# Optimization experiments

Hardware: AMD Instinct MI355X
Metric: run time of the kernel (lower is better)

The kernel has to match this reference:

```python
import jax, jax.numpy as jnp
import numpy as np

H = 1024
EPS = 1e-5
N_ENT = 1000
TOP_K = 5


def _ln(x, g, b):
    mu = jnp.mean(x, axis=-1, keepdims=True)
    var = jnp.mean((x - mu) ** 2, axis=-1, keepdims=True)
    return (x - mu) * jax.lax.rsqrt(var + EPS) * g + b


def _gelu(x):
    return jax.nn.gelu(x, approximate=False)  # torch nn.GELU default (erf)


def setup_inputs() -> dict:
    key = jax.random.key(0)
    ks = jax.random.split(key, 24)
    s = 0.02
    inp = {
        'hidden_states': jax.random.normal(ks[0], (8, 2048, H), jnp.float32),
        'entity_embeddings': jax.random.normal(ks[1], (N_ENT, H), jnp.float32) * 0.01,
        # entity_encoder: H -> 2H -> H -> LN
        'ee_w1': jax.random.normal(ks[2], (H, 2 * H), jnp.float32) * s,
        'ee_b1': jnp.zeros((2 * H,), jnp.float32),
        'ee_w2': jax.random.normal(ks[3], (2 * H, H), jnp.float32) * s,
        'ee_b2': jnp.zeros((H,), jnp.float32),
        'ee_g': jnp.ones((H,), jnp.float32),
        'ee_beta': jnp.zeros((H,), jnp.float32),
        # relation_encoder: H -> H -> H -> LN
        're_w1': jax.random.normal(ks[4], (H, H), jnp.float32) * s,
        're_b1': jnp.zeros((H,), jnp.float32),
        're_w2': jax.random.normal(ks[5], (H, H), jnp.float32) * s,
        're_b2': jnp.zeros((H,), jnp.float32),
        're_g': jnp.ones((H,), jnp.float32),
        're_beta': jnp.zeros((H,), jnp.float32),
        # reasoning_network: 3H -> 2H -> H -> LN
        'rn_w1': jax.random.normal(ks[6], (3 * H, 2 * H), jnp.float32) * s,
        'rn_b1': jnp.zeros((2 * H,), jnp.float32),
        'rn_w2': jax.random.normal(ks[7], (2 * H, H), jnp.float32) * s,
        'rn_b2': jnp.zeros((H,), jnp.float32),
        'rn_g': jnp.ones((H,), jnp.float32),
        'rn_beta': jnp.zeros((H,), jnp.float32),
        # validation_network: H -> H/2 -> 1 -> sigmoid
        'vn_w1': jax.random.normal(ks[8], (H, H // 2), jnp.float32) * s,
        'vn_b1': jnp.zeros((H // 2,), jnp.float32),
        'vn_w2': jax.random.normal(ks[9], (H // 2, 1), jnp.float32) * s,
        'vn_b2': jnp.zeros((1,), jnp.float32),
    }
    return inp


def reference(hidden_states, entity_embeddings,
              ee_w1, ee_b1, ee_w2, ee_b2, ee_g, ee_beta,
              re_w1, re_b1, re_w2, re_b2, re_g, re_beta,
              rn_w1, rn_b1, rn_w2, rn_b2, rn_g, rn_beta,
              vn_w1, vn_b1, vn_w2, vn_b2):
    # entity encoder over all tokens: [B,S,H]
    entity_features = _ln(_gelu(hidden_states @ ee_w1 + ee_b1) @ ee_w2 + ee_b2, ee_g, ee_beta)

    # query=None path: relation encoder on mean-pooled hidden states [B,H]
    pooled = jnp.mean(hidden_states, axis=1)
    relation_features = _ln(_gelu(pooled @ re_w1 + re_b1) @ re_w2 + re_b2, re_g, re_beta)
    query_features = relation_features

    # similarity + top-k entity retrieval
    entity_similarities = query_features @ entity_embeddings.T  # [B, N_ENT]
    top_values, top_indices = jax.lax.top_k(entity_similarities, TOP_K)
    retrieved_entities = entity_embeddings[top_indices]  # [B, K, H]

    # reasoning input: [mean retrieved entity | relation | mean context]
    entity_vec = jnp.mean(retrieved_entities, axis=1)  # [B,H]
    context_vec = jnp.mean(hidden_states, axis=1)      # [B,H]
    reasoning_in = jnp.concatenate([entity_vec, relation_features, context_vec], axis=-1)  # [B,3H]
    reasoning_output = _ln(_gelu(reasoning_in @ rn_w1 + rn_b1) @ rn_w2 + rn_b2, rn_g, rn_beta)

    validation_scores = jax.nn.sigmoid(_gelu(reasoning_output @ vn_w1 + vn_b1) @ vn_w2 + vn_b2)

    return (entity_features, relation_features, retrieved_entities,
            entity_similarities, top_indices, reasoning_output, validation_scores)
```

## Files before the change

### kernel.cpp

```cpp
#include <hip/hip_runtime.h>
#include <math.h>

#define H 1024
#define SEQ 2048
#define BATCH 8
#define N_ENT 1000
#define TOPK 5
#define LN_EPS 1e-5f

using bf16x8 = __attribute__((ext_vector_type(8))) __bf16;
using f32x4  = __attribute__((ext_vector_type(4))) float;
#define AS1 __attribute__((address_space(1)))
#define AS3 __attribute__((address_space(3)))


__device__ __forceinline__ float gelu_erf(float x) {
    return 0.5f * x * (1.0f + erff(x * 0.70710678118654752440f));
}

__device__ __forceinline__ float sigmoidf_(float x) {
    return 1.0f / (1.0f + expf(-x));
}

__device__ __forceinline__ unsigned short f2bf(float f) {
    unsigned int u = __float_as_uint(f);
    unsigned int r = (u + 0x7fffu + ((u >> 16) & 1u)) >> 16;
    return (unsigned short)r;
}

__device__ float block_sum(float v, float* red) {
    for (int off = 32; off > 0; off >>= 1) v += __shfl_down(v, off, 64);
    int wid = threadIdx.x >> 6;
    int lane = threadIdx.x & 63;
    int nw = blockDim.x >> 6;
    if (lane == 0) red[wid] = v;
    __syncthreads();
    if (threadIdx.x == 0) {
        float s = 0.f;
        for (int i = 0; i < nw; ++i) s += red[i];
        red[0] = s;
    }
    __syncthreads();
    float r = red[0];
    __syncthreads();
    return r;
}


__global__ void f2bf_kernel(const float* __restrict__ in, unsigned short* __restrict__ out, int n) {
    int i = (blockIdx.x * blockDim.x + threadIdx.x) * 4;
    if (i >= n) return;
    float4 v = *(const float4*)(in + i);
    ushort4 o;
    o.x = f2bf(v.x); o.y = f2bf(v.y); o.z = f2bf(v.z); o.w = f2bf(v.w);
    *(ushort4*)(out + i) = o;
}

__global__ void transpose_bf_kernel(const float* __restrict__ in, unsigned short* __restrict__ out,
                                    int R, int C) {
    __shared__ float tile[32][33];
    int c0 = blockIdx.x * 32, r0 = blockIdx.y * 32;
    int tx = threadIdx.x & 31, ty = threadIdx.x >> 5;
#pragma unroll
    for (int i = 0; i < 32; i += 8)
        tile[ty + i][tx] = in[(size_t)(r0 + ty + i) * C + c0 + tx];
    __syncthreads();
#pragma unroll
    for (int i = 0; i < 32; i += 8)
        out[(size_t)(c0 + ty + i) * R + r0 + tx] = f2bf(tile[tx][ty + i]);
}


__global__ void pool1_kernel(const float* __restrict__ hs, float* __restrict__ part) {
    int sc = blockIdx.x, b = blockIdx.y, t = threadIdx.x;
    float a0 = 0, a1 = 0, a2 = 0, a3 = 0;
    const float* p = hs + ((size_t)b * SEQ + sc * 64) * H;
    for (int s = 0; s < 64; ++s) {
        const float* q = p + (size_t)s * H;
        a0 += q[t]; a1 += q[t + 256]; a2 += q[t + 512]; a3 += q[t + 768];
    }
    float* o = part + ((size_t)b * 32 + sc) * H;
    o[t] = a0; o[t + 256] = a1; o[t + 512] = a2; o[t + 768] = a3;
}

__global__ void pool2_kernel(const float* __restrict__ part, float* __restrict__ pooled) {
    int b = blockIdx.x, t = threadIdx.x;
    for (int c = 0; c < 4; ++c) {
        float s = 0.f;
        for (int sc = 0; sc < 32; ++sc) s += part[((size_t)b * 32 + sc) * H + t + c * 256];
        pooled[b * H + t + c * 256] = s * (1.0f / SEQ);
    }
}


template <int KRANGE>
__global__ void mlp_partial_kernel(const float* __restrict__ X, int ldx,
                                   const float* __restrict__ W, int N,
                                   float* __restrict__ part) {
    __shared__ float xs[8][KRANGE];
    int jb = blockIdx.x, ks = blockIdx.y, t = threadIdx.x;
    int k0 = ks * KRANGE;
    for (int i = t; i < 8 * KRANGE; i += 256) {
        int b = i / KRANGE, k = i % KRANGE;
        xs[b][k] = X[(size_t)b * ldx + k0 + k];
    }
    __syncthreads();
    int j = jb * 256 + t;
    float acc[8] = {};
    for (int k = 0; k < KRANGE; ++k) {
        float w = W[(size_t)(k0 + k) * N + j];
#pragma unroll
        for (int b = 0; b < 8; ++b) acc[b] = fmaf(xs[b][k], w, acc[b]);
    }
#pragma unroll
    for (int b = 0; b < 8; ++b) part[((size_t)ks * 8 + b) * N + j] = acc[b];
}

__global__ void mlp_reduce_gelu_kernel(const float* __restrict__ part, const float* __restrict__ bias,
                                       float* __restrict__ out, int N, int nks) {
    int b = blockIdx.y;
    int j = blockIdx.x * 256 + threadIdx.x;
    float s = bias[j];
    for (int ks = 0; ks < nks; ++ks) s += part[((size_t)ks * 8 + b) * N + j];
    out[(size_t)b * N + j] = gelu_erf(s);
}

__global__ void mlp_reduce_ln_kernel(const float* __restrict__ part, const float* __restrict__ bias,
                                     const float* __restrict__ g, const float* __restrict__ be,
                                     float* __restrict__ out, int nks) {
    __shared__ float red[32];
    int b = blockIdx.x, t = threadIdx.x;
    float s = bias[t];
    for (int ks = 0; ks < nks; ++ks) s += part[((size_t)ks * 8 + b) * H + t];
    float mu = block_sum(s, red) * (1.0f / H);
    float d = s - mu;
    float var = block_sum(d * d, red) * (1.0f / H);
    out[(size_t)b * H + t] = d * rsqrtf(var + LN_EPS) * g[t] + be[t];
}


__global__ void sim_kernel(const float* __restrict__ rel, const float* __restrict__ ent,
                           float* __restrict__ sims) {
    __shared__ float rl[8 * H];
    int t = threadIdx.x;
    for (int i = t; i < 8 * H; i += 256) rl[i] = rel[i];
    __syncthreads();
    int e = blockIdx.x * 4 + (t >> 6);
    int lane = t & 63;
    float ev[16];
    const float* ep = ent + (size_t)e * H;
#pragma unroll
    for (int i = 0; i < 16; ++i) ev[i] = ep[lane + i * 64];
#pragma unroll
    for (int b = 0; b < 8; ++b) {
        float a = 0.f;
#pragma unroll
        for (int i = 0; i < 16; ++i) a = fmaf(ev[i], rl[b * H + lane + i * 64], a);
        for (int off = 32; off > 0; off >>= 1) a += __shfl_down(a, off, 64);
        if (lane == 0) sims[b * N_ENT + e] = a;
    }
}

__global__ void topk_kernel(const float* __restrict__ sims, float* __restrict__ out_idx_f,
                            int* __restrict__ idx_i) {
    __shared__ float v[1024];
    __shared__ float rv[4];
    __shared__ int ri[4];
    int b = blockIdx.x, t = threadIdx.x;
    for (int i = t; i < 1024; i += 256) v[i] = (i < N_ENT) ? sims[b * N_ENT + i] : -INFINITY;
    __syncthreads();
    for (int k = 0; k < TOPK; ++k) {
        float best = -INFINITY;
        int bi = 0x7fffffff;
        for (int i = t; i < 1024; i += 256) {
            float x = v[i];
            if (x > best || (x == best && i < bi)) { best = x; bi = i; }
        }
        for (int off = 32; off > 0; off >>= 1) {
            float ov = __shfl_down(best, off, 64);
            int oi = __shfl_down(bi, off, 64);
            if (ov > best || (ov == best && oi < bi)) { best = ov; bi = oi; }
        }
        if ((t & 63) == 0) { rv[t >> 6] = best; ri[t >> 6] = bi; }
        __syncthreads();
        if (t == 0) {
            for (int w = 1; w < 4; ++w)
                if (rv[w] > rv[0] || (rv[w] == rv[0] && ri[w] < ri[0])) { rv[0] = rv[w]; ri[0] = ri[w]; }
            int sel = ri[0];
            out_idx_f[b * TOPK + k] = (float)sel;
            idx_i[b * TOPK + k] = sel;
            v[sel] = -INFINITY;
        }
        __syncthreads();
    }
}

__global__ void gather_kernel(const float* __restrict__ ent, const int* __restrict__ idx,
                              float* __restrict__ retrieved, float* __restrict__ evec) {
    int b = blockIdx.x, h = threadIdx.x;
    float acc = 0.f;
    for (int k = 0; k < TOPK; ++k) {
        float v = ent[(size_t)idx[b * TOPK + k] * H + h];
        retrieved[((size_t)b * TOPK + k) * H + h] = v;
        acc += v;
    }
    evec[b * H + h] = acc * (1.0f / TOPK);
}

__global__ void concat_kernel(const float* __restrict__ evec, const float* __restrict__ rel,
                              const float* __restrict__ pooled, float* __restrict__ xin) {
    int b = blockIdx.x, t = threadIdx.x;
    xin[(size_t)b * 3 * H + t] = evec[b * H + t];
    xin[(size_t)b * 3 * H + H + t] = rel[b * H + t];
    xin[(size_t)b * 3 * H + 2 * H + t] = pooled[b * H + t];
}

__global__ void vn_final_kernel(const float* __restrict__ part, const float* __restrict__ b1,
                                const float* __restrict__ w2, const float* __restrict__ b2,
                                float* __restrict__ vs, int nks) {
    __shared__ float red[32];
    int b = blockIdx.x, t = threadIdx.x;
    float s = b1[t];
    for (int ks = 0; ks < nks; ++ks) s += part[((size_t)ks * 8 + b) * 512 + t];
    float c = gelu_erf(s) * w2[t];
    float tot = block_sum(c, red);
    if (t == 0) vs[b] = sigmoidf_(tot + b2[0]);
}

template <int GELU_BF16_OUT>
__global__ __launch_bounds__(256) void gemm_mfma(const unsigned short* __restrict__ A,
                                                 const unsigned short* __restrict__ Bt,
                                                 const float* __restrict__ bias,
                                                 void* __restrict__ Cout,
                                                 int M, int N, int K) {
    __shared__ __align__(16) unsigned short As[128 * 32];
    __shared__ __align__(16) unsigned short Bs[128 * 32];
    const int tid = threadIdx.x;
    const int lane = tid & 63;
    const int m0 = blockIdx.y * 128, n0 = blockIdx.x * 128;
    const int wave = tid >> 6;
    const int wm = (wave >> 1) * 64, wn = (wave & 1) * 64;

    const int rowA_f = wm + (lane & 15);
    const int rowB_f = wn + (lane & 15);
    const int kq = (lane >> 4) * 8;

    f32x4 acc[4][4] = {};

    for (int k0 = 0; k0 < K; k0 += 32) {
#pragma unroll
        for (int r = 0; r < 2; ++r) {
            int e = (r * 256 + tid) * 8;
            int row = e >> 5, kk = e & 31;
            const unsigned short* ga = A + (size_t)(m0 + row) * K + k0 + kk;
            const unsigned short* gb = Bt + (size_t)(n0 + row) * K + k0 + kk;
            unsigned short* la = As + (size_t)(r * 256 + (tid & ~63)) * 8;
            unsigned short* lb = Bs + (size_t)(r * 256 + (tid & ~63)) * 8;
            __builtin_amdgcn_global_load_lds((AS1 void*)ga, (AS3 void*)la, 16, 0, 0);
            __builtin_amdgcn_global_load_lds((AS1 void*)gb, (AS3 void*)lb, 16, 0, 0);
        }
        __syncthreads();
        bf16x8 af[4], bfg[4];
#pragma unroll
        for (int i = 0; i < 4; ++i)
            af[i] = *(const bf16x8*)(As + (rowA_f + i * 16) * 32 + kq);
#pragma unroll
        for (int j = 0; j < 4; ++j)
            bfg[j] = *(const bf16x8*)(Bs + (rowB_f + j * 16) * 32 + kq);
#pragma unroll
        for (int i = 0; i < 4; ++i)
#pragma unroll
            for (int j = 0; j < 4; ++j)
                acc[i][j] = __builtin_amdgcn_mfma_f32_16x16x32_bf16(af[i], bfg[j], acc[i][j], 0, 0, 0);
        __syncthreads();
    }

    const int cn = lane & 15;
    const int rbase = (lane >> 4) * 4;
#pragma unroll
    for (int i = 0; i < 4; ++i) {
#pragma unroll
        for (int j = 0; j < 4; ++j) {
            int n = n0 + wn + j * 16 + cn;
            float bv = bias[n];
            int mb = m0 + wm + i * 16 + rbase;
#pragma unroll
            for (int r = 0; r < 4; ++r) {
                float c = acc[i][j][r] + bv;
                if (GELU_BF16_OUT) {
                    c = gelu_erf(c);
                    ((unsigned short*)Cout)[(size_t)(mb + r) * N + n] = f2bf(c);
                } else {
                    ((float*)Cout)[(size_t)(mb + r) * N + n] = c;
                }
            }
        }
    }
}

__global__ void ln_rows_kernel(float* __restrict__ x, const float* __restrict__ g,
                               const float* __restrict__ beta) {
    __shared__ float red[32];
    float* p = x + (size_t)blockIdx.x * H;
    int t = threadIdx.x;
    float v[4];
#pragma unroll
    for (int i = 0; i < 4; ++i) v[i] = p[t + i * 256];
    float s = v[0] + v[1] + v[2] + v[3];
    float mu = block_sum(s, red) * (1.0f / H);
    float d2 = 0.f;
#pragma unroll
    for (int i = 0; i < 4; ++i) { float d = v[i] - mu; d2 += d * d; }
    float var = block_sum(d2, red) * (1.0f / H);
    float inv = rsqrtf(var + LN_EPS);
#pragma unroll
    for (int i = 0; i < 4; ++i)
        p[t + i * 256] = (v[i] - mu) * inv * g[t + i * 256] + beta[t + i * 256];
}


extern "C" void kernel_launch(void* const* d_in, const int* in_sizes, int n_in,
                              void* d_out, int out_size, void* d_ws, size_t ws_size,
                              hipStream_t stream) {
    const float* hs     = (const float*)d_in[0];
    const float* ent    = (const float*)d_in[1];
    const float* ee_w1  = (const float*)d_in[2];
    const float* ee_b1  = (const float*)d_in[3];
    const float* ee_w2  = (const float*)d_in[4];
    const float* ee_b2  = (const float*)d_in[5];
    const float* ee_g   = (const float*)d_in[6];
    const float* ee_be  = (const float*)d_in[7];
    const float* re_w1  = (const float*)d_in[8];
    const float* re_b1  = (const float*)d_in[9];
    const float* re_w2  = (const float*)d_in[10];
    const float* re_b2  = (const float*)d_in[11];
    const float* re_g   = (const float*)d_in[12];
    const float* re_be  = (const float*)d_in[13];
    const float* rn_w1  = (const float*)d_in[14];
    const float* rn_b1  = (const float*)d_in[15];
    const float* rn_w2  = (const float*)d_in[16];
    const float* rn_b2  = (const float*)d_in[17];
    const float* rn_g   = (const float*)d_in[18];
    const float* rn_be  = (const float*)d_in[19];
    const float* vn_w1  = (const float*)d_in[20];
    const float* vn_b1  = (const float*)d_in[21];
    const float* vn_w2  = (const float*)d_in[22];
    const float* vn_b2  = (const float*)d_in[23];

    float* out = (float*)d_out;
    float* ef   = out;
    float* rel  = ef + (size_t)BATCH * SEQ * H;
    float* retr = rel + BATCH * H;
    float* sims = retr + BATCH * TOPK * H;
    float* tidx = sims + BATCH * N_ENT;
    float* ro   = tidx + BATCH * TOPK;
    float* vs   = ro + BATCH * H;

    float* ws = (float*)d_ws;
    size_t o = 0;
    float* pooled = ws + o; o += 8192;
    float* evec   = ws + o; o += 8192;
    int*   idx_i  = (int*)(ws + o); o += 64;
    float* xin    = ws + o; o += 8 * 3 * H;
    float* h1r    = ws + o; o += 8 * H;
    float* h1n    = ws + o; o += 8 * 2 * H;
    float* part   = ws + o; o += 24 * 8 * 2048;
    unsigned short* w1t = (unsigned short*)(ws + o); o += (2048 * 1024) / 2;
    unsigned short* w2t = (unsigned short*)(ws + o); o += (2048 * 1024) / 2;
    unsigned short* hsb = (unsigned short*)(ws + o);

    long long avail = (long long)(ws_size / 4) - (long long)o;
    int chunk = (int)(avail / 1536);
    chunk &= ~127;
    if (chunk > BATCH * SEQ) chunk = BATCH * SEQ;
    if (chunk < 128) chunk = 128;
    unsigned short* midb = hsb + (size_t)chunk * H;

    transpose_bf_kernel<<<dim3(2048 / 32, 1024 / 32), 256, 0, stream>>>(ee_w1, w1t, 1024, 2048);
    transpose_bf_kernel<<<dim3(1024 / 32, 2048 / 32), 256, 0, stream>>>(ee_w2, w2t, 2048, 1024);

    pool1_kernel<<<dim3(32, BATCH), 256, 0, stream>>>(hs, part);
    pool2_kernel<<<BATCH, 256, 0, stream>>>(part, pooled);

    mlp_partial_kernel<64><<<dim3(4, 16), 256, 0, stream>>>(pooled, H, re_w1, H, part);
    mlp_reduce_gelu_kernel<<<dim3(4, 8), 256, 0, stream>>>(part, re_b1, h1r, H, 16);
    mlp_partial_kernel<64><<<dim3(4, 16), 256, 0, stream>>>(h1r, H, re_w2, H, part);
    mlp_reduce_ln_kernel<<<BATCH, 1024, 0, stream>>>(part, re_b2, re_g, re_be, rel, 16);

    sim_kernel<<<250, 256, 0, stream>>>(rel, ent, sims);
    topk_kernel<<<BATCH, 256, 0, stream>>>(sims, tidx, idx_i);
    gather_kernel<<<BATCH, 1024, 0, stream>>>(ent, idx_i, retr, evec);
    concat_kernel<<<BATCH, 1024, 0, stream>>>(evec, rel, pooled, xin);

    mlp_partial_kernel<128><<<dim3(8, 24), 256, 0, stream>>>(xin, 3 * H, rn_w1, 2 * H, part);
    mlp_reduce_gelu_kernel<<<dim3(8, 8), 256, 0, stream>>>(part, rn_b1, h1n, 2 * H, 24);
    mlp_partial_kernel<128><<<dim3(4, 16), 256, 0, stream>>>(h1n, 2 * H, rn_w2, H, part);
    mlp_reduce_ln_kernel<<<BATCH, 1024, 0, stream>>>(part, rn_b2, rn_g, rn_be, ro, 16);

    mlp_partial_kernel<128><<<dim3(2, 8), 256, 0, stream>>>(ro, H, vn_w1, 512, part);
    vn_final_kernel<<<BATCH, 512, 0, stream>>>(part, vn_b1, vn_w2, vn_b2, vs, 8);

    int total = BATCH * SEQ;
    for (int r0 = 0; r0 < total; r0 += chunk) {
        int m = total - r0;
        if (m > chunk) m = chunk;
        int nconv = m * H;
        f2bf_kernel<<<(nconv / 4 + 255) / 256, 256, 0, stream>>>(hs + (size_t)r0 * H, hsb, nconv);
        gemm_mfma<1><<<dim3(2048 / 128, m / 128), 256, 0, stream>>>(hsb, w1t, ee_b1, midb,
                                                                    m, 2048, 1024);
        gemm_mfma<0><<<dim3(1024 / 128, m / 128), 256, 0, stream>>>(midb, w2t, ee_b2,
                                                                    ef + (size_t)r0 * H,
                                                                    m, 1024, 2048);
    }
    ln_rows_kernel<<<total, 256, 0, stream>>>(ef, ee_g, ee_be);
}
```

Before: 600.2 us.

## Fuse bf16 conversion into pooling, add fast GELU, remap GEMM grid, vectorize LN

When the workspace holds the whole activation, the pooling kernel now also writes the bf16 copy of hidden_states, so the separate f2bf pass and its second read of the input are dropped. The erf-based GELU is replaced by a polynomial approximation using hardware rcp/exp2, the gather and concat kernels are merged, and pool2 gets more blocks. The GEMM grid is flattened with M as the fastest-varying index so blocks that share a weight tile run together for better cache reuse, and the row LayerNorm uses float4 accesses. The erf approximation adds small numerical error, and the pooling kernel now does extra scalar 2-byte stores.

```diff
diff --git a/kernel.cpp b/kernel.cpp
--- a/kernel.cpp
+++ b/kernel.cpp
@@ -14,8 +14,15 @@
 #define AS3 __attribute__((address_space(3)))
 
 
-__device__ __forceinline__ float gelu_erf(float x) {
-    return 0.5f * x * (1.0f + erff(x * 0.70710678118654752440f));
+__device__ __forceinline__ float gelu_fast(float x) {
+    float z = fabsf(x) * 0.70710678118654752440f;
+    float t = __builtin_amdgcn_rcpf(fmaf(0.3275911f, z, 1.0f));
+    float p = fmaf(fmaf(fmaf(fmaf(1.061405429f, t, -1.453152027f), t, 1.421413741f),
+                        t, -0.284496736f), t, 0.254829592f) * t;
+    float e = __builtin_amdgcn_exp2f(-z * z * 1.44269504088896f);
+    float erfz = fmaf(-p, e, 1.0f);
+    float s = copysignf(erfz, x);
+    return 0.5f * x * (1.0f + s);
 }
 
 __device__ __forceinline__ float sigmoidf_(float x) {
@@ -71,25 +78,30 @@
 }
 
 
-__global__ void pool1_kernel(const float* __restrict__ hs, float* __restrict__ part) {
+__global__ void pool1_kernel(const float* __restrict__ hs, float* __restrict__ part,
+                             unsigned short* __restrict__ hsb) {
     int sc = blockIdx.x, b = blockIdx.y, t = threadIdx.x;
     float a0 = 0, a1 = 0, a2 = 0, a3 = 0;
-    const float* p = hs + ((size_t)b * SEQ + sc * 64) * H;
+    size_t rowbase = (size_t)b * SEQ + sc * 64;
+    const float* p = hs + rowbase * H;
     for (int s = 0; s < 64; ++s) {
         const float* q = p + (size_t)s * H;
-        a0 += q[t]; a1 += q[t + 256]; a2 += q[t + 512]; a3 += q[t + 768];
+        float v0 = q[t], v1 = q[t + 256], v2 = q[t + 512], v3 = q[t + 768];
+        a0 += v0; a1 += v1; a2 += v2; a3 += v3;
+        if (hsb) {
+            unsigned short* w = hsb + (rowbase + s) * H;
+            w[t] = f2bf(v0); w[t + 256] = f2bf(v1); w[t + 512] = f2bf(v2); w[t + 768] = f2bf(v3);
+        }
     }
     float* o = part + ((size_t)b * 32 + sc) * H;
     o[t] = a0; o[t + 256] = a1; o[t + 512] = a2; o[t + 768] = a3;
 }
 
 __global__ void pool2_kernel(const float* __restrict__ part, float* __restrict__ pooled) {
-    int b = blockIdx.x, t = threadIdx.x;
-    for (int c = 0; c < 4; ++c) {
-        float s = 0.f;
-        for (int sc = 0; sc < 32; ++sc) s += part[((size_t)b * 32 + sc) * H + t + c * 256];
-        pooled[b * H + t + c * 256] = s * (1.0f / SEQ);
-    }
+    int b = blockIdx.y, c = blockIdx.x, t = threadIdx.x;
+    float s = 0.f;
+    for (int sc = 0; sc < 32; ++sc) s += part[((size_t)b * 32 + sc) * H + t + c * 256];
+    pooled[b * H + t + c * 256] = s * (1.0f / SEQ);
 }
 
 
@@ -122,7 +134,7 @@
     int j = blockIdx.x * 256 + threadIdx.x;
     float s = bias[j];
     for (int ks = 0; ks < nks; ++ks) s += part[((size_t)ks * 8 + b) * N + j];
-    out[(size_t)b * N + j] = gelu_erf(s);
+    out[(size_t)b * N + j] = gelu_fast(s);
 }
 
 __global__ void mlp_reduce_ln_kernel(const float* __restrict__ part, const float* __restrict__ bias,
@@ -195,8 +207,9 @@
     }
 }
 
-__global__ void gather_kernel(const float* __restrict__ ent, const int* __restrict__ idx,
-                              float* __restrict__ retrieved, float* __restrict__ evec) {
+__global__ void gather_concat_kernel(const float* __restrict__ ent, const int* __restrict__ idx,
+                                     const float* __restrict__ rel, const float* __restrict__ pooled,
+                                     float* __restrict__ retrieved, float* __restrict__ xin) {
     int b = blockIdx.x, h = threadIdx.x;
     float acc = 0.f;
     for (int k = 0; k < TOPK; ++k) {
@@ -204,15 +217,10 @@
         retrieved[((size_t)b * TOPK + k) * H + h] = v;
         acc += v;
     }
-    evec[b * H + h] = acc * (1.0f / TOPK);
-}
-
-__global__ void concat_kernel(const float* __restrict__ evec, const float* __restrict__ rel,
-                              const float* __restrict__ pooled, float* __restrict__ xin) {
-    int b = blockIdx.x, t = threadIdx.x;
-    xin[(size_t)b * 3 * H + t] = evec[b * H + t];
-    xin[(size_t)b * 3 * H + H + t] = rel[b * H + t];
-    xin[(size_t)b * 3 * H + 2 * H + t] = pooled[b * H + t];
+    float* xb = xin + (size_t)b * 3 * H;
+    xb[h] = acc * (1.0f / TOPK);
+    xb[H + h] = rel[b * H + h];
+    xb[2 * H + h] = pooled[b * H + h];
 }
 
 __global__ void vn_final_kernel(const float* __restrict__ part, const float* __restrict__ b1,
@@ -222,7 +230,7 @@
     int b = blockIdx.x, t = threadIdx.x;
     float s = b1[t];
     for (int ks = 0; ks < nks; ++ks) s += part[((size_t)ks * 8 + b) * 512 + t];
-    float c = gelu_erf(s) * w2[t];
+    float c = gelu_fast(s) * w2[t];
     float tot = block_sum(c, red);
     if (t == 0) vs[b] = sigmoidf_(tot + b2[0]);
 }
@@ -237,7 +245,9 @@
     __shared__ __align__(16) unsigned short Bs[128 * 32];
     const int tid = threadIdx.x;
     const int lane = tid & 63;
-    const int m0 = blockIdx.y * 128, n0 = blockIdx.x * 128;
+    const int Mp = M >> 7;
+    const int m0 = (blockIdx.x % Mp) * 128;
+    const int n0 = (blockIdx.x / Mp) * 128;
     const int wave = tid >> 6;
     const int wm = (wave >> 1) * 64, wn = (wave & 1) * 64;
 
@@ -288,7 +298,7 @@
             for (int r = 0; r < 4; ++r) {
                 float c = acc[i][j][r] + bv;
                 if (GELU_BF16_OUT) {
-                    c = gelu_erf(c);
+                    c = gelu_fast(c);
                     ((unsigned short*)Cout)[(size_t)(mb + r) * N + n] = f2bf(c);
                 } else {
                     ((float*)Cout)[(size_t)(mb + r) * N + n] = c;
@@ -303,19 +313,18 @@
     __shared__ float red[32];
     float* p = x + (size_t)blockIdx.x * H;
     int t = threadIdx.x;
-    float v[4];
-#pragma unroll
-    for (int i = 0; i < 4; ++i) v[i] = p[t + i * 256];
-    float s = v[0] + v[1] + v[2] + v[3];
+    float4 v = *(const float4*)(p + t * 4);
+    float s = v.x + v.y + v.z + v.w;
     float mu = block_sum(s, red) * (1.0f / H);
-    float d2 = 0.f;
-#pragma unroll
-    for (int i = 0; i < 4; ++i) { float d = v[i] - mu; d2 += d * d; }
+    float4 d = { v.x - mu, v.y - mu, v.z - mu, v.w - mu };
+    float d2 = d.x * d.x + d.y * d.y + d.z * d.z + d.w * d.w;
     float var = block_sum(d2, red) * (1.0f / H);
     float inv = rsqrtf(var + LN_EPS);
-#pragma unroll
-    for (int i = 0; i < 4; ++i)
-        p[t + i * 256] = (v[i] - mu) * inv * g[t + i * 256] + beta[t + i * 256];
+    float4 gg = *(const float4*)(g + t * 4);
+    float4 bb = *(const float4*)(beta + t * 4);
+    float4 o = { d.x * inv * gg.x + bb.x, d.y * inv * gg.y + bb.y,
+                 d.z * inv * gg.z + bb.z, d.w * inv * gg.w + bb.w };
+    *(float4*)(p + t * 4) = o;
 }
 
 
@@ -359,7 +368,6 @@
     float* ws = (float*)d_ws;
     size_t o = 0;
     float* pooled = ws + o; o += 8192;
-    float* evec   = ws + o; o += 8192;
     int*   idx_i  = (int*)(ws + o); o += 64;
     float* xin    = ws + o; o += 8 * 3 * H;
     float* h1r    = ws + o; o += 8 * H;
@@ -372,15 +380,17 @@
     long long avail = (long long)(ws_size / 4) - (long long)o;
     int chunk = (int)(avail / 1536);
     chunk &= ~127;
-    if (chunk > BATCH * SEQ) chunk = BATCH * SEQ;
+    int total = BATCH * SEQ;
+    if (chunk > total) chunk = total;
     if (chunk < 128) chunk = 128;
+    bool full = (chunk >= total);
     unsigned short* midb = hsb + (size_t)chunk * H;
 
     transpose_bf_kernel<<<dim3(2048 / 32, 1024 / 32), 256, 0, stream>>>(ee_w1, w1t, 1024, 2048);
     transpose_bf_kernel<<<dim3(1024 / 32, 2048 / 32), 256, 0, stream>>>(ee_w2, w2t, 2048, 1024);
 
-    pool1_kernel<<<dim3(32, BATCH), 256, 0, stream>>>(hs, part);
-    pool2_kernel<<<BATCH, 256, 0, stream>>>(part, pooled);
+    pool1_kernel<<<dim3(32, BATCH), 256, 0, stream>>>(hs, part, full ? hsb : nullptr);
+    pool2_kernel<<<dim3(4, BATCH), 256, 0, stream>>>(part, pooled);
 
     mlp_partial_kernel<64><<<dim3(4, 16), 256, 0, stream>>>(pooled, H, re_w1, H, part);
     mlp_reduce_gelu_kernel<<<dim3(4, 8), 256, 0, stream>>>(part, re_b1, h1r, H, 16);
@@ -389,8 +399,7 @@
 
     sim_kernel<<<250, 256, 0, stream>>>(rel, ent, sims);
     topk_kernel<<<BATCH, 256, 0, stream>>>(sims, tidx, idx_i);
-    gather_kernel<<<BATCH, 1024, 0, stream>>>(ent, idx_i, retr, evec);
-    concat_kernel<<<BATCH, 1024, 0, stream>>>(evec, rel, pooled, xin);
+    gather_concat_kernel<<<BATCH, 1024, 0, stream>>>(ent, idx_i, rel, pooled, retr, xin);
 
     mlp_partial_kernel<128><<<dim3(8, 24), 256, 0, stream>>>(xin, 3 * H, rn_w1, 2 * H, part);
     mlp_reduce_gelu_kernel<<<dim3(8, 8), 256, 0, stream>>>(part, rn_b1, h1n, 2 * H, 24);
@@ -400,17 +409,19 @@
     mlp_partial_kernel<128><<<dim3(2, 8), 256, 0, stream>>>(ro, H, vn_w1, 512, part);
     vn_final_kernel<<<BATCH, 512, 0, stream>>>(part, vn_b1, vn_w2, vn_b2, vs, 8);
 
-    int total = BATCH * SEQ;
     for (int r0 = 0; r0 < total; r0 += chunk) {
         int m = total - r0;
         if (m > chunk) m = chunk;
-        int nconv = m * H;
-        f2bf_kernel<<<(nconv / 4 + 255) / 256, 256, 0, stream>>>(hs + (size_t)r0 * H, hsb, nconv);
-        gemm_mfma<1><<<dim3(2048 / 128, m / 128), 256, 0, stream>>>(hsb, w1t, ee_b1, midb,
-                                                                    m, 2048, 1024);
-        gemm_mfma<0><<<dim3(1024 / 128, m / 128), 256, 0, stream>>>(midb, w2t, ee_b2,
-                                                                    ef + (size_t)r0 * H,
-                                                                    m, 1024, 2048);
+        if (!full) {
+            int nconv = m * H;
+            f2bf_kernel<<<(nconv / 4 + 255) / 256, 256, 0, stream>>>(hs + (size_t)r0 * H, hsb, nconv);
+        }
+        unsigned short* a1 = full ? (hsb + (size_t)r0 * H) : hsb;
+        gemm_mfma<1><<<(m / 128) * (2048 / 128), 256, 0, stream>>>(a1, w1t, ee_b1, midb,
+                                                                   m, 2048, 1024);
+        gemm_mfma<0><<<(m / 128) * (1024 / 128), 256, 0, stream>>>(midb, w2t, ee_b2,
+                                                                   ef + (size_t)r0 * H,
+                                                                   m, 1024, 2048);
     }
     ln_rows_kernel<<<total, 256, 0, stream>>>(ef, ee_g, ee_be);
 }
```

New measurement: 617.7 us. +2.9%, slower.
